# Optimization experiments

Measured on AMD Instinct MI355X. Metric: run time of the kernel, lower is better.

The kernel has to match this reference:

```python
import jax, jax.numpy as jnp
import numpy as np

CURV_BOUNDS = (-2.0, 2.0)
THRESH = 0.01   # |k| below this -> Euclidean branch
EPS = 1e-5

B, S, D = 4, 2048, 512


def setup_inputs() -> dict:
    key = jax.random.key(0)
    ks = jax.random.split(key, 8)
    x = jax.random.normal(ks[0], (B, S, D), jnp.float32)
    sc = 1.0 / np.sqrt(D)  # ~ nn.Linear default init scale
    Wq = jax.random.uniform(ks[1], (D, D), jnp.float32, -sc, sc)
    bq = jax.random.uniform(ks[2], (D,), jnp.float32, -sc, sc)
    Wk = jax.random.uniform(ks[3], (D, D), jnp.float32, -sc, sc)
    bk = jax.random.uniform(ks[4], (D,), jnp.float32, -sc, sc)
    Wv = jax.random.uniform(ks[5], (D, D), jnp.float32, -sc, sc)
    bv = jax.random.uniform(ks[6], (D,), jnp.float32, -sc, sc)
    curvature_raw = jnp.float32(0.5)   # init_curvature
    temperature = jnp.float32(1.0)
    mask = jnp.triu(jnp.ones((S, S), dtype=bool), 1)  # causal: True = masked out
    return {"x": x, "Wq": Wq, "bq": bq, "Wk": Wk, "bk": bk, "Wv": Wv,
            "bv": bv, "curvature_raw": curvature_raw,
            "temperature": temperature, "mask": mask}


def _curvature(raw):
    k_min, k_max = CURV_BOUNDS
    return k_min + (k_max - k_min) * (jnp.tanh(raw) + 1.0) / 2.0


def _project(u, k):
    # project_to_manifold: identity (euclid), Poincare-ball clip (k<0), sphere renorm (k>0)
    n = jnp.sqrt(jnp.sum(u * u, axis=-1, keepdims=True) + 1e-12)
    absk = jnp.abs(k)
    sk = jnp.sqrt(jnp.maximum(absk, EPS))
    max_norm = (1.0 - 1e-3) / sk                      # ball radius 1/sqrt(|k|)
    u_hyp = u * jnp.minimum(1.0, max_norm / n)
    u_sph = u / (n * sk)                              # sphere radius 1/sqrt(k)
    return jnp.where(absk < THRESH, u, jnp.where(k < 0, u_hyp, u_sph))


def reference(x, Wq, bq, Wk, bk, Wv, bv, curvature_raw, temperature, mask):
    k = _curvature(curvature_raw)
    q = x @ Wq.T + bq
    kk = x @ Wk.T + bk
    v = x @ Wv.T + bv
    qm = _project(q, k)
    km = _project(kk, k)

    # pairwise quantities without materializing [B,S,S,D]
    dots = jnp.einsum('bid,bjd->bij', qm, km)         # [B,S,S]
    qn2 = jnp.sum(qm * qm, axis=-1)                   # [B,S]
    kn2 = jnp.sum(km * km, axis=-1)                   # [B,S]
    diff2 = jnp.maximum(qn2[:, :, None] + kn2[:, None, :] - 2.0 * dots, 0.0)

    absk = jnp.abs(k)
    sk = jnp.sqrt(jnp.maximum(absk, EPS))

    d_euc = jnp.sqrt(diff2 + 1e-12)
    # hyperbolic (Poincare ball, c=|k|): acosh(1 + 2c|x-y|^2 / ((1-c|x|^2)(1-c|y|^2))) / sqrt(c)
    denom = jnp.maximum((1.0 - absk * qn2)[:, :, None] * (1.0 - absk * kn2)[:, None, :], EPS)
    arg = 1.0 + 2.0 * absk * diff2 / denom
    d_hyp = jnp.arccosh(jnp.maximum(arg, 1.0 + 1e-7)) / sk
    # spherical (radius 1/sqrt(k)): arccos(k * <x,y>) / sqrt(k)
    cosang = jnp.clip(absk * dots, -1.0 + 1e-7, 1.0 - 1e-7)
    d_sph = jnp.arccos(cosang) / sk

    dist = jnp.where(absk < THRESH, d_euc, jnp.where(k < 0, d_hyp, d_sph))

    scores = -dist / (temperature + 1e-8)
    scores = jnp.where(mask[None, :, :], -jnp.inf, scores)
    attention = jax.nn.softmax(scores, axis=-1)       # [B,S,S]
    output = jnp.einsum('bij,bjd->bid', attention, v) # [B,S,D]
    return output, attention
```

## Files before the change

### kernel.cpp

```cpp
#include <hip/hip_runtime.h>
#include <hip/hip_bf16.h>
#include <math.h>

typedef unsigned short u16;
typedef float float4e __attribute__((ext_vector_type(4)));
typedef short short8 __attribute__((ext_vector_type(8)));
typedef unsigned short ushort8 __attribute__((ext_vector_type(8)));
typedef unsigned short u16x4 __attribute__((ext_vector_type(4)));

#define SEQ 2048
#define DIM 512
#define NB  4

__device__ __forceinline__ float bf2f(u16 h) {
    return __uint_as_float(((unsigned)h) << 16);
}
__device__ __forceinline__ u16 f2bf(float f) {
    __hip_bfloat16 h = __float2bfloat16(f);
    return *reinterpret_cast<u16*>(&h);
}
__device__ __forceinline__ float curv_of(float raw) {
    return -2.0f + 2.0f * (tanhf(raw) + 1.0f);
}
__device__ __forceinline__ void gl_lds16(const u16* g, u16* lds) {
    __builtin_amdgcn_global_load_lds(
        (const __attribute__((address_space(1))) unsigned int*)g,
        (__attribute__((address_space(3))) unsigned int*)lds, 16, 0, 0);
}

__global__ __launch_bounds__(256) void cvt_all_kernel(
    const float* __restrict__ x, const float* __restrict__ Wq,
    const float* __restrict__ Wk, const float* __restrict__ Wv,
    u16* __restrict__ x_bf, u16* __restrict__ Wcat, float* __restrict__ lsum,
    float* __restrict__ outz)
{
    const int n_x = NB * SEQ * DIM, n_w = DIM * DIM;
    const int n_out = NB * SEQ * DIM;
    int gid = blockIdx.x * 256 + threadIdx.x;
    if (gid < NB * SEQ) lsum[gid] = 0.f;
    if (gid < n_out / 4) ((float4*)outz)[gid] = (float4){0.f, 0.f, 0.f, 0.f};
    int i4 = gid * 4;
    if (i4 < n_x) {
        float4 v = *(const float4*)&x[i4];
        u16x4 h = {f2bf(v.x), f2bf(v.y), f2bf(v.z), f2bf(v.w)};
        *(u16x4*)&x_bf[i4] = h;
    } else if (i4 < n_x + 3 * n_w) {
        int j = i4 - n_x;
        const float* W = (j < n_w) ? Wq : (j < 2 * n_w ? Wk : Wv);
        int off = j % n_w;
        float4 v = *(const float4*)&W[off];
        u16x4 h = {f2bf(v.x), f2bf(v.y), f2bf(v.z), f2bf(v.w)};
        *(u16x4*)&Wcat[j] = h;
    }
}

template<int MODE>
__global__ __launch_bounds__(256, 8) void gemm64_kernel(
    const u16* __restrict__ A, int lda, long long sA,
    const u16* __restrict__ Bt, int ldb, long long sB,
    void* __restrict__ Cv, int ldc, long long sC,
    u16* __restrict__ vT,
    float* __restrict__ lsum,
    const float* __restrict__ bq, const float* __restrict__ bk, const float* __restrict__ bv,
    const float* __restrict__ qn2v, const float* __restrict__ kn2v,
    const float* __restrict__ curvp, const float* __restrict__ tempp)
{
    int bx = blockIdx.x, bm = blockIdx.y, b = blockIdx.z;
    int bn = (MODE == 2) ? (bx & 7) : bx;
    int kp = (MODE == 2) ? (bx >> 3) : 0;
    if (MODE == 1 && bn > bm) return;

    __shared__ __align__(16) u16 As[64 * 64];
    __shared__ __align__(16) u16 Bs[64 * 64];

    int t = threadIdx.x, wave = t >> 6, lane = t & 63;
    int wr = wave >> 1, wc = wave & 1;
    int lrow = lane & 15, quad = lane >> 4;
    int srow = lane >> 3, sc = lane & 7;

    const u16* Ab = A + (size_t)b * sA + (size_t)(bm * 64) * lda;
    const u16* Bb = Bt + (size_t)b * sB + (size_t)(bn * 64) * ldb;

    float4e acc[2][2];
#pragma unroll
    for (int i = 0; i < 2; i++)
#pragma unroll
        for (int j = 0; j < 2; j++) acc[i][j] = (float4e){0.f, 0.f, 0.f, 0.f};

    int ktBeg = (MODE == 2) ? kp : 0;
    int ktEnd = (MODE == 2) ? (bm + 1) : 8;
    int ktStp = (MODE == 2) ? 2 : 1;

    for (int kt = ktBeg; kt < ktEnd; kt += ktStp) {
        int k0 = kt << 6;
        __syncthreads();
#pragma unroll
        for (int h = 0; h < 2; ++h) {
            int q = wave * 2 + h;
            int row = q * 8 + srow;
            int c = sc ^ (row & 7);
            gl_lds16(Ab + (size_t)row * lda + k0 + c * 8, &As[q * 512]);
            gl_lds16(Bb + (size_t)row * ldb + k0 + c * 8, &Bs[q * 512]);
        }
        __syncthreads();
#pragma unroll
        for (int s = 0; s < 2; ++s) {
            short8 af[2], bfr[2];
#pragma unroll
            for (int im = 0; im < 2; im++) {
                int R = wr * 32 + im * 16 + lrow;
                af[im] = *(const short8*)&As[R * 64 + (((s * 4 + quad) ^ (R & 7)) * 8)];
            }
#pragma unroll
            for (int in = 0; in < 2; in++) {
                int R = wc * 32 + in * 16 + lrow;
                bfr[in] = *(const short8*)&Bs[R * 64 + (((s * 4 + quad) ^ (R & 7)) * 8)];
            }
#pragma unroll
            for (int im = 0; im < 2; im++)
#pragma unroll
                for (int in = 0; in < 2; in++)
                    acc[im][in] = __builtin_amdgcn_mfma_f32_16x16x32_bf16(af[im], bfr[in], acc[im][in], 0, 0, 0);
        }
    }

    if (MODE == 0) {
        u16* Cb = (u16*)Cv;
#pragma unroll
        for (int im = 0; im < 2; im++)
#pragma unroll
            for (int in = 0; in < 2; in++) {
                int gi0 = bm * 64 + wr * 32 + im * 16 + quad * 4;
                int gj = bn * 64 + wc * 32 + in * 16 + lrow;
                float bias = (gj < 512) ? bq[gj] : (gj < 1024 ? bk[gj - 512] : bv[gj - 1024]);
                u16x4 pack;
#pragma unroll
                for (int r = 0; r < 4; r++) {
                    u16 hv = f2bf(acc[im][in][r] + bias);
                    Cb[(size_t)(gi0 + r) * ldc + gj] = hv;
                    pack[r] = hv;
                }
                if (gj >= 1024) {
                    int bb = gi0 >> 11, s = gi0 & 2047;
                    *(u16x4*)&vT[((size_t)bb * DIM + (gj - 1024)) * SEQ + s] = pack;
                }
            }
    } else if (MODE == 1) {
        float kv = curv_of(curvp[0]);
        float absk = fabsf(kv);
        float sk = sqrtf(fmaxf(absk, 1e-5f));
        float invT = 1.0f / (tempp[0] + 1e-8f);
        u16* Cb = (u16*)Cv + (size_t)b * sC;

        float psum[2][4];
#pragma unroll
        for (int im = 0; im < 2; im++)
#pragma unroll
            for (int r = 0; r < 4; r++) psum[im][r] = 0.f;

#pragma unroll
        for (int im = 0; im < 2; im++) {
#pragma unroll
            for (int r = 0; r < 4; r++) {
                int gi = bm * 64 + wr * 32 + im * 16 + quad * 4 + r;
                float qn = qn2v[b * SEQ + gi];
#pragma unroll
                for (int in = 0; in < 2; in++) {
                    int gj = bn * 64 + wc * 32 + in * 16 + lrow;
                    float kn = kn2v[b * SEQ + gj];
                    float dot = acc[im][in][r];
                    float diff2 = fmaxf(qn + kn - 2.f * dot, 0.f);
                    float dist;
                    if (absk < 0.01f) {
                        dist = sqrtf(diff2 + 1e-12f);
                    } else if (kv < 0.f) {
                        float denom = fmaxf((1.f - absk * qn) * (1.f - absk * kn), 1e-5f);
                        float arg = fmaxf(1.f + 2.f * absk * diff2 / denom, 1.f + 1e-7f);
                        dist = acoshf(arg) / sk;
                    } else {
                        float c = fminf(fmaxf(absk * dot, -1.f + 1e-7f), 1.f - 1e-7f);
                        dist = acosf(c) / sk;
                    }
                    float s = -dist * invT;
                    float e = (gj <= gi) ? __expf(s) : 0.f;
                    Cb[(size_t)gi * ldc + gj] = f2bf(e);
                    psum[im][r] += e;
                }
            }
        }
#pragma unroll
        for (int im = 0; im < 2; im++)
#pragma unroll
            for (int r = 0; r < 4; r++) {
                float v = psum[im][r];
                v += __shfl_xor(v, 1);
                v += __shfl_xor(v, 2);
                v += __shfl_xor(v, 4);
                v += __shfl_xor(v, 8);
                if (lrow == 0) {
                    int gi = bm * 64 + wr * 32 + im * 16 + quad * 4 + r;
                    atomicAdd(&lsum[b * SEQ + gi], v);
                }
            }
    } else {
        float* Cb = (float*)Cv + (size_t)b * sC;
#pragma unroll
        for (int im = 0; im < 2; im++)
#pragma unroll
            for (int r = 0; r < 4; r++) {
                int gi = bm * 64 + wr * 32 + im * 16 + quad * 4 + r;
                float invl = 1.0f / lsum[b * SEQ + gi];
#pragma unroll
                for (int in = 0; in < 2; in++) {
                    int gd = bn * 64 + wc * 32 + in * 16 + lrow;
                    atomicAdd(&Cb[(size_t)gi * ldc + gd], acc[im][in][r] * invl);
                }
            }
    }
}

__global__ __launch_bounds__(256) void project_kernel(
    const u16* __restrict__ qkvh,
    u16* __restrict__ qm, u16* __restrict__ km,
    float* __restrict__ qn2, float* __restrict__ kn2,
    const float* __restrict__ curvp)
{
    int wave = threadIdx.x >> 6, lane = threadIdx.x & 63;
    int r = blockIdx.x * 4 + wave;
    float kv = curv_of(curvp[0]);
    float absk = fabsf(kv);
    float sk = sqrtf(fmaxf(absk, 1e-5f));

    const u16* qrow = qkvh + (size_t)r * 1536;
    ushort8 qh = *(const ushort8*)&qrow[lane * 8];
    ushort8 kh = *(const ushort8*)&qrow[512 + lane * 8];

    float qv[8], kw[8];
    float sq = 0.f, s2 = 0.f;
#pragma unroll
    for (int e = 0; e < 8; e++) {
        qv[e] = bf2f(qh[e]); sq += qv[e] * qv[e];
        kw[e] = bf2f(kh[e]); s2 += kw[e] * kw[e];
    }
#pragma unroll
    for (int off = 1; off < 64; off <<= 1) {
        sq += __shfl_xor(sq, off);
        s2 += __shfl_xor(s2, off);
    }

    float sclq, sclk;
    {
        float nq = sqrtf(sq + 1e-12f);
        float nk = sqrtf(s2 + 1e-12f);
        if (absk < 0.01f) { sclq = 1.f; sclk = 1.f; }
        else if (kv < 0.f) {
            float mx = (1.0f - 1e-3f) / sk;
            sclq = fminf(1.f, mx / nq);
            sclk = fminf(1.f, mx / nk);
        } else {
            sclq = 1.f / (nq * sk);
            sclk = 1.f / (nk * sk);
        }
    }
    if (lane == 0) {
        qn2[r] = sq * sclq * sclq;
        kn2[r] = s2 * sclk * sclk;
    }
    ushort8 qo, ko;
#pragma unroll
    for (int e = 0; e < 8; e++) {
        qo[e] = f2bf(qv[e] * sclq);
        ko[e] = f2bf(kw[e] * sclk);
    }
    *(ushort8*)&qm[(size_t)r * 512 + lane * 8] = qo;
    *(ushort8*)&km[(size_t)r * 512 + lane * 8] = ko;
}

__global__ __launch_bounds__(256) void norm_attn_kernel(
    const u16* __restrict__ attnH, const float* __restrict__ lsum,
    float* __restrict__ attnF)
{
    int i = blockIdx.x, b = blockIdx.y, t = threadIdx.x;
    float inv = 1.0f / lsum[b * SEQ + i];
    const u16* rowh = attnH + ((size_t)b * SEQ + i) * SEQ;
    float* row = attnF + ((size_t)b * SEQ + i) * SEQ;
    int L = i + 1;
    int j0 = t * 8;
    float4 lo, hi;
    if (j0 + 8 <= L) {
        ushort8 h = *(const ushort8*)&rowh[j0];
        lo.x = bf2f(h[0]) * inv; lo.y = bf2f(h[1]) * inv;
        lo.z = bf2f(h[2]) * inv; lo.w = bf2f(h[3]) * inv;
        hi.x = bf2f(h[4]) * inv; hi.y = bf2f(h[5]) * inv;
        hi.z = bf2f(h[6]) * inv; hi.w = bf2f(h[7]) * inv;
    } else {
        float v[8];
#pragma unroll
        for (int e = 0; e < 8; e++)
            v[e] = (j0 + e < L) ? bf2f(rowh[j0 + e]) * inv : 0.f;
        lo = (float4){v[0], v[1], v[2], v[3]};
        hi = (float4){v[4], v[5], v[6], v[7]};
    }
    *(float4*)&row[j0] = lo;
    *(float4*)&row[j0 + 4] = hi;
}

extern "C" void kernel_launch(void* const* d_in, const int* in_sizes, int n_in,
                              void* d_out, int out_size, void* d_ws, size_t ws_size,
                              hipStream_t stream) {
    (void)in_sizes; (void)n_in; (void)out_size; (void)ws_size;

    const float* x    = (const float*)d_in[0];
    const float* Wq   = (const float*)d_in[1];
    const float* bq   = (const float*)d_in[2];
    const float* Wk   = (const float*)d_in[3];
    const float* bk   = (const float*)d_in[4];
    const float* Wv   = (const float*)d_in[5];
    const float* bv   = (const float*)d_in[6];
    const float* curv = (const float*)d_in[7];
    const float* temp = (const float*)d_in[8];

    float* out   = (float*)d_out;
    float* attnF = out + (size_t)NB * SEQ * DIM;

    char* ws = (char*)d_ws;
    u16*   x_bf  = (u16*)(ws + 0);
    u16*   Wcat  = (u16*)(ws + 8388608);
    u16*   qkvh  = (u16*)(ws + 9961472);
    u16*   qm    = (u16*)(ws + 35127296);
    u16*   km    = (u16*)(ws + 43515904);
    u16*   vT    = (u16*)(ws + 51904512);
    float* qn2   = (float*)(ws + 60293120);
    float* kn2   = (float*)(ws + 60325888);
    float* lsum  = (float*)(ws + 60358656);
    u16*   attnH = (u16*)(ws + 0);

    {
        int n_tot = (NB * SEQ * DIM + 3 * DIM * DIM) / 4;
        cvt_all_kernel<<<(n_tot + 255) / 256, 256, 0, stream>>>(x, Wq, Wk, Wv, x_bf, Wcat, lsum, out);
    }

    gemm64_kernel<0><<<dim3(1536 / 64, 8192 / 64, 1), 256, 0, stream>>>(
        x_bf, 512, 0, Wcat, 512, 0, (void*)qkvh, 1536, 0,
        vT, nullptr, bq, bk, bv, nullptr, nullptr, nullptr, nullptr);

    project_kernel<<<NB * SEQ / 4, 256, 0, stream>>>(qkvh, qm, km, qn2, kn2, curv);

    gemm64_kernel<1><<<dim3(SEQ / 64, SEQ / 64, NB), 256, 0, stream>>>(
        qm, 512, (long long)SEQ * DIM, km, 512, (long long)SEQ * DIM,
        (void*)attnH, SEQ, (long long)SEQ * SEQ,
        nullptr, lsum, nullptr, nullptr, nullptr, qn2, kn2, curv, temp);

    gemm64_kernel<2><<<dim3(2 * DIM / 64, SEQ / 64, NB), 256, 0, stream>>>(
        attnH, SEQ, (long long)SEQ * SEQ, vT, SEQ, (long long)DIM * SEQ,
        (void*)out, DIM, (long long)SEQ * DIM,
        nullptr, lsum, nullptr, nullptr, nullptr, nullptr, nullptr, nullptr, nullptr);

    norm_attn_kernel<<<dim3(SEQ, NB), 256, 0, stream>>>(attnH, lsum, attnF);
}
```

Before: 239.4 us.

## Switch GEMMs to 128x128 tiles with 32-wide K steps and add fast acos

```diff
diff --git a/kernel.cpp b/kernel.cpp
--- a/kernel.cpp
+++ b/kernel.cpp
@@ -21,6 +21,12 @@
 }
 __device__ __forceinline__ float curv_of(float raw) {
     return -2.0f + 2.0f * (tanhf(raw) + 1.0f);
+}
+__device__ __forceinline__ float fast_acos(float x) {
+    float ax = fabsf(x);
+    float r = sqrtf(fmaxf(1.f - ax, 0.f)) *
+              (1.5707288f + ax * (-0.2121144f + ax * (0.0742610f - 0.0187293f * ax)));
+    return (x < 0.f) ? (3.14159265f - r) : r;
 }
 __device__ __forceinline__ void gl_lds16(const u16* g, u16* lds) {
     __builtin_amdgcn_global_load_lds(
@@ -55,7 +61,7 @@
 }
 
 template<int MODE>
-__global__ __launch_bounds__(256, 8) void gemm64_kernel(
+__global__ __launch_bounds__(256) void gemm128_kernel(
     const u16* __restrict__ A, int lda, long long sA,
     const u16* __restrict__ Bt, int ldb, long long sB,
     void* __restrict__ Cv, int ldc, long long sC,
@@ -66,72 +72,69 @@
     const float* __restrict__ curvp, const float* __restrict__ tempp)
 {
     int bx = blockIdx.x, bm = blockIdx.y, b = blockIdx.z;
-    int bn = (MODE == 2) ? (bx & 7) : bx;
-    int kp = (MODE == 2) ? (bx >> 3) : 0;
+    int bn = (MODE == 2) ? (bx & 3) : bx;
+    int kp = (MODE == 2) ? (bx >> 2) : 0;
     if (MODE == 1 && bn > bm) return;
 
-    __shared__ __align__(16) u16 As[64 * 64];
-    __shared__ __align__(16) u16 Bs[64 * 64];
+    __shared__ __align__(16) u16 As[128 * 32];
+    __shared__ __align__(16) u16 Bs[128 * 32];
 
     int t = threadIdx.x, wave = t >> 6, lane = t & 63;
-    int wr = wave >> 1, wc = wave & 1;
+    int wm = wave >> 1, wn = wave & 1;
     int lrow = lane & 15, quad = lane >> 4;
-    int srow = lane >> 3, sc = lane & 7;
-
-    const u16* Ab = A + (size_t)b * sA + (size_t)(bm * 64) * lda;
-    const u16* Bb = Bt + (size_t)b * sB + (size_t)(bn * 64) * ldb;
-
-    float4e acc[2][2];
-#pragma unroll
-    for (int i = 0; i < 2; i++)
-#pragma unroll
-        for (int j = 0; j < 2; j++) acc[i][j] = (float4e){0.f, 0.f, 0.f, 0.f};
+    int srow = lane >> 2, sch = lane & 3;
+
+    const u16* Ab = A + (size_t)b * sA + (size_t)(bm * 128) * lda;
+    const u16* Bb = Bt + (size_t)b * sB + (size_t)(bn * 128) * ldb;
+
+    float4e acc[4][4];
+#pragma unroll
+    for (int i = 0; i < 4; i++)
+#pragma unroll
+        for (int j = 0; j < 4; j++) acc[i][j] = (float4e){0.f, 0.f, 0.f, 0.f};
 
     int ktBeg = (MODE == 2) ? kp : 0;
-    int ktEnd = (MODE == 2) ? (bm + 1) : 8;
+    int ktEnd = (MODE == 2) ? ((bm + 1) * 4) : 16;
     int ktStp = (MODE == 2) ? 2 : 1;
 
     for (int kt = ktBeg; kt < ktEnd; kt += ktStp) {
-        int k0 = kt << 6;
+        int k0 = kt << 5;
         __syncthreads();
 #pragma unroll
         for (int h = 0; h < 2; ++h) {
-            int q = wave * 2 + h;
-            int row = q * 8 + srow;
-            int c = sc ^ (row & 7);
-            gl_lds16(Ab + (size_t)row * lda + k0 + c * 8, &As[q * 512]);
-            gl_lds16(Bb + (size_t)row * ldb + k0 + c * 8, &Bs[q * 512]);
+            int row = wave * 16 + srow + h * 64;
+            int c = sch ^ (row & 3);
+            gl_lds16(Ab + (size_t)row * lda + k0 + c * 8, &As[(wave * 16 + h * 64) * 32]);
+            gl_lds16(Bb + (size_t)row * ldb + k0 + c * 8, &Bs[(wave * 16 + h * 64) * 32]);
         }
         __syncthreads();
-#pragma unroll
-        for (int s = 0; s < 2; ++s) {
-            short8 af[2], bfr[2];
-#pragma unroll
-            for (int im = 0; im < 2; im++) {
-                int R = wr * 32 + im * 16 + lrow;
-                af[im] = *(const short8*)&As[R * 64 + (((s * 4 + quad) ^ (R & 7)) * 8)];
-            }
-#pragma unroll
-            for (int in = 0; in < 2; in++) {
-                int R = wc * 32 + in * 16 + lrow;
-                bfr[in] = *(const short8*)&Bs[R * 64 + (((s * 4 + quad) ^ (R & 7)) * 8)];
-            }
-#pragma unroll
-            for (int im = 0; im < 2; im++)
-#pragma unroll
-                for (int in = 0; in < 2; in++)
-                    acc[im][in] = __builtin_amdgcn_mfma_f32_16x16x32_bf16(af[im], bfr[in], acc[im][in], 0, 0, 0);
-        }
+
+        short8 af[4], bfr[4];
+#pragma unroll
+        for (int im = 0; im < 4; im++) {
+            int R = wm * 64 + im * 16 + lrow;
+            af[im] = *(const short8*)&As[R * 32 + ((quad ^ (R & 3)) * 8)];
+        }
+#pragma unroll
+        for (int in = 0; in < 4; in++) {
+            int R = wn * 64 + in * 16 + lrow;
+            bfr[in] = *(const short8*)&Bs[R * 32 + ((quad ^ (R & 3)) * 8)];
+        }
+#pragma unroll
+        for (int im = 0; im < 4; im++)
+#pragma unroll
+            for (int in = 0; in < 4; in++)
+                acc[im][in] = __builtin_amdgcn_mfma_f32_16x16x32_bf16(af[im], bfr[in], acc[im][in], 0, 0, 0);
     }
 
     if (MODE == 0) {
         u16* Cb = (u16*)Cv;
 #pragma unroll
-        for (int im = 0; im < 2; im++)
-#pragma unroll
-            for (int in = 0; in < 2; in++) {
-                int gi0 = bm * 64 + wr * 32 + im * 16 + quad * 4;
-                int gj = bn * 64 + wc * 32 + in * 16 + lrow;
+        for (int im = 0; im < 4; im++)
+#pragma unroll
+            for (int in = 0; in < 4; in++) {
+                int gi0 = bm * 128 + wm * 64 + im * 16 + quad * 4;
+                int gj = bn * 128 + wn * 64 + in * 16 + lrow;
                 float bias = (gj < 512) ? bq[gj] : (gj < 1024 ? bk[gj - 512] : bv[gj - 1024]);
                 u16x4 pack;
 #pragma unroll
@@ -149,24 +152,25 @@
         float kv = curv_of(curvp[0]);
         float absk = fabsf(kv);
         float sk = sqrtf(fmaxf(absk, 1e-5f));
+        float invsk = 1.0f / sk;
         float invT = 1.0f / (tempp[0] + 1e-8f);
         u16* Cb = (u16*)Cv + (size_t)b * sC;
 
-        float psum[2][4];
-#pragma unroll
-        for (int im = 0; im < 2; im++)
+        float psum[4][4];
+#pragma unroll
+        for (int im = 0; im < 4; im++)
 #pragma unroll
             for (int r = 0; r < 4; r++) psum[im][r] = 0.f;
 
 #pragma unroll
-        for (int im = 0; im < 2; im++) {
+        for (int im = 0; im < 4; im++) {
 #pragma unroll
             for (int r = 0; r < 4; r++) {
-                int gi = bm * 64 + wr * 32 + im * 16 + quad * 4 + r;
+                int gi = bm * 128 + wm * 64 + im * 16 + quad * 4 + r;
                 float qn = qn2v[b * SEQ + gi];
 #pragma unroll
-                for (int in = 0; in < 2; in++) {
-                    int gj = bn * 64 + wc * 32 + in * 16 + lrow;
+                for (int in = 0; in < 4; in++) {
+                    int gj = bn * 128 + wn * 64 + in * 16 + lrow;
                     float kn = kn2v[b * SEQ + gj];
                     float dot = acc[im][in][r];
                     float diff2 = fmaxf(qn + kn - 2.f * dot, 0.f);
@@ -176,10 +180,10 @@
                     } else if (kv < 0.f) {
                         float denom = fmaxf((1.f - absk * qn) * (1.f - absk * kn), 1e-5f);
                         float arg = fmaxf(1.f + 2.f * absk * diff2 / denom, 1.f + 1e-7f);
-                        dist = acoshf(arg) / sk;
+                        dist = acoshf(arg) * invsk;
                     } else {
                         float c = fminf(fmaxf(absk * dot, -1.f + 1e-7f), 1.f - 1e-7f);
-                        dist = acosf(c) / sk;
+                        dist = fast_acos(c) * invsk;
                     }
                     float s = -dist * invT;
                     float e = (gj <= gi) ? __expf(s) : 0.f;
@@ -189,7 +193,7 @@
             }
         }
 #pragma unroll
-        for (int im = 0; im < 2; im++)
+        for (int im = 0; im < 4; im++)
 #pragma unroll
             for (int r = 0; r < 4; r++) {
                 float v = psum[im][r];
@@ -198,21 +202,21 @@
                 v += __shfl_xor(v, 4);
                 v += __shfl_xor(v, 8);
                 if (lrow == 0) {
-                    int gi = bm * 64 + wr * 32 + im * 16 + quad * 4 + r;
+                    int gi = bm * 128 + wm * 64 + im * 16 + quad * 4 + r;
                     atomicAdd(&lsum[b * SEQ + gi], v);
                 }
             }
     } else {
         float* Cb = (float*)Cv + (size_t)b * sC;
 #pragma unroll
-        for (int im = 0; im < 2; im++)
+        for (int im = 0; im < 4; im++)
 #pragma unroll
             for (int r = 0; r < 4; r++) {
-                int gi = bm * 64 + wr * 32 + im * 16 + quad * 4 + r;
+                int gi = bm * 128 + wm * 64 + im * 16 + quad * 4 + r;
                 float invl = 1.0f / lsum[b * SEQ + gi];
 #pragma unroll
-                for (int in = 0; in < 2; in++) {
-                    int gd = bn * 64 + wc * 32 + in * 16 + lrow;
+                for (int in = 0; in < 4; in++) {
+                    int gd = bn * 128 + wn * 64 + in * 16 + lrow;
                     atomicAdd(&Cb[(size_t)gi * ldc + gd], acc[im][in][r] * invl);
                 }
             }
@@ -340,18 +344,18 @@
         cvt_all_kernel<<<(n_tot + 255) / 256, 256, 0, stream>>>(x, Wq, Wk, Wv, x_bf, Wcat, lsum, out);
     }
 
-    gemm64_kernel<0><<<dim3(1536 / 64, 8192 / 64, 1), 256, 0, stream>>>(
+    gemm128_kernel<0><<<dim3(1536 / 128, 8192 / 128, 1), 256, 0, stream>>>(
         x_bf, 512, 0, Wcat, 512, 0, (void*)qkvh, 1536, 0,
         vT, nullptr, bq, bk, bv, nullptr, nullptr, nullptr, nullptr);
 
     project_kernel<<<NB * SEQ / 4, 256, 0, stream>>>(qkvh, qm, km, qn2, kn2, curv);
 
-    gemm64_kernel<1><<<dim3(SEQ / 64, SEQ / 64, NB), 256, 0, stream>>>(
+    gemm128_kernel<1><<<dim3(SEQ / 128, SEQ / 128, NB), 256, 0, stream>>>(
         qm, 512, (long long)SEQ * DIM, km, 512, (long long)SEQ * DIM,
         (void*)attnH, SEQ, (long long)SEQ * SEQ,
         nullptr, lsum, nullptr, nullptr, nullptr, qn2, kn2, curv, temp);
 
-    gemm64_kernel<2><<<dim3(2 * DIM / 64, SEQ / 64, NB), 256, 0, stream>>>(
+    gemm128_kernel<2><<<dim3(2 * DIM / 128, SEQ / 128, NB), 256, 0, stream>>>(
         attnH, SEQ, (long long)SEQ * SEQ, vT, SEQ, (long long)DIM * SEQ,
         (void*)out, DIM, (long long)SEQ * DIM,
         nullptr, lsum, nullptr, nullptr, nullptr, nullptr, nullptr, nullptr, nullptr);
```

Measured after the change: 279.9 us. 1.17x slower.

## Fuse fp32-to-bf16 conversion into QKV GEMM and drop split-K atomics in PV

Applied to the files above, without the earlier changes.

```diff
diff --git a/kernel.cpp b/kernel.cpp
--- a/kernel.cpp
+++ b/kernel.cpp
@@ -22,36 +22,105 @@
 __device__ __forceinline__ float curv_of(float raw) {
     return -2.0f + 2.0f * (tanhf(raw) + 1.0f);
 }
+__device__ __forceinline__ float fast_acos(float x) {
+    float ax = fabsf(x);
+    float r = sqrtf(fmaxf(1.f - ax, 0.f)) *
+              (1.5707288f + ax * (-0.2121144f + ax * (0.0742610f - 0.0187293f * ax)));
+    return (x < 0.f) ? (3.14159265f - r) : r;
+}
 __device__ __forceinline__ void gl_lds16(const u16* g, u16* lds) {
     __builtin_amdgcn_global_load_lds(
         (const __attribute__((address_space(1))) unsigned int*)g,
         (__attribute__((address_space(3))) unsigned int*)lds, 16, 0, 0);
 }
 
-__global__ __launch_bounds__(256) void cvt_all_kernel(
-    const float* __restrict__ x, const float* __restrict__ Wq,
-    const float* __restrict__ Wk, const float* __restrict__ Wv,
-    u16* __restrict__ x_bf, u16* __restrict__ Wcat, float* __restrict__ lsum,
-    float* __restrict__ outz)
+__global__ __launch_bounds__(256, 4) void qkv_kernel(
+    const float* __restrict__ xf,
+    const float* __restrict__ Wq, const float* __restrict__ Wk, const float* __restrict__ Wv,
+    const float* __restrict__ bq, const float* __restrict__ bk, const float* __restrict__ bv,
+    u16* __restrict__ C, u16* __restrict__ vT)
 {
-    const int n_x = NB * SEQ * DIM, n_w = DIM * DIM;
-    const int n_out = NB * SEQ * DIM;
-    int gid = blockIdx.x * 256 + threadIdx.x;
-    if (gid < NB * SEQ) lsum[gid] = 0.f;
-    if (gid < n_out / 4) ((float4*)outz)[gid] = (float4){0.f, 0.f, 0.f, 0.f};
-    int i4 = gid * 4;
-    if (i4 < n_x) {
-        float4 v = *(const float4*)&x[i4];
-        u16x4 h = {f2bf(v.x), f2bf(v.y), f2bf(v.z), f2bf(v.w)};
-        *(u16x4*)&x_bf[i4] = h;
-    } else if (i4 < n_x + 3 * n_w) {
-        int j = i4 - n_x;
-        const float* W = (j < n_w) ? Wq : (j < 2 * n_w ? Wk : Wv);
-        int off = j % n_w;
-        float4 v = *(const float4*)&W[off];
-        u16x4 h = {f2bf(v.x), f2bf(v.y), f2bf(v.z), f2bf(v.w)};
-        *(u16x4*)&Wcat[j] = h;
-    }
+    int bn = blockIdx.x, bm = blockIdx.y;
+
+    __shared__ __align__(16) u16 As[64 * 64];
+    __shared__ __align__(16) u16 Bs[64 * 64];
+
+    int t = threadIdx.x, wave = t >> 6, lane = t & 63;
+    int wr = wave >> 1, wc = wave & 1;
+    int lrow = lane & 15, quad = lane >> 4;
+    int srow = lane >> 3, sc = lane & 7;
+
+    const float* Af = xf + (size_t)(bm * 64) * 512;
+    const float* Wsel = (bn < 8) ? Wq : (bn < 16 ? Wk : Wv);
+    const float* Bf = Wsel + (size_t)((bn & 7) * 64) * 512;
+
+    float4e acc[2][2];
+#pragma unroll
+    for (int i = 0; i < 2; i++)
+#pragma unroll
+        for (int j = 0; j < 2; j++) acc[i][j] = (float4e){0.f, 0.f, 0.f, 0.f};
+
+    for (int kt = 0; kt < 8; ++kt) {
+        int k0 = kt << 6;
+        __syncthreads();
+#pragma unroll
+        for (int h = 0; h < 2; ++h) {
+            int q = wave * 2 + h;
+            int row = q * 8 + srow;
+            int c = sc ^ srow;
+            const float* ga = Af + (size_t)row * 512 + k0 + c * 8;
+            float4 a0 = *(const float4*)ga, a1 = *(const float4*)(ga + 4);
+            const float* gb = Bf + (size_t)row * 512 + k0 + c * 8;
+            float4 b0 = *(const float4*)gb, b1 = *(const float4*)(gb + 4);
+            ushort8 ha, hb;
+            ha[0] = f2bf(a0.x); ha[1] = f2bf(a0.y); ha[2] = f2bf(a0.z); ha[3] = f2bf(a0.w);
+            ha[4] = f2bf(a1.x); ha[5] = f2bf(a1.y); ha[6] = f2bf(a1.z); ha[7] = f2bf(a1.w);
+            hb[0] = f2bf(b0.x); hb[1] = f2bf(b0.y); hb[2] = f2bf(b0.z); hb[3] = f2bf(b0.w);
+            hb[4] = f2bf(b1.x); hb[5] = f2bf(b1.y); hb[6] = f2bf(b1.z); hb[7] = f2bf(b1.w);
+            *(ushort8*)&As[(size_t)row * 64 + sc * 8] = ha;
+            *(ushort8*)&Bs[(size_t)row * 64 + sc * 8] = hb;
+        }
+        __syncthreads();
+#pragma unroll
+        for (int s = 0; s < 2; ++s) {
+            short8 af[2], bfr[2];
+#pragma unroll
+            for (int im = 0; im < 2; im++) {
+                int R = wr * 32 + im * 16 + lrow;
+                af[im] = *(const short8*)&As[R * 64 + (((s * 4 + quad) ^ (R & 7)) * 8)];
+            }
+#pragma unroll
+            for (int in = 0; in < 2; in++) {
+                int R = wc * 32 + in * 16 + lrow;
+                bfr[in] = *(const short8*)&Bs[R * 64 + (((s * 4 + quad) ^ (R & 7)) * 8)];
+            }
+#pragma unroll
+            for (int im = 0; im < 2; im++)
+#pragma unroll
+                for (int in = 0; in < 2; in++)
+                    acc[im][in] = __builtin_amdgcn_mfma_f32_16x16x32_bf16(af[im], bfr[in], acc[im][in], 0, 0, 0);
+        }
+    }
+
+#pragma unroll
+    for (int im = 0; im < 2; im++)
+#pragma unroll
+        for (int in = 0; in < 2; in++) {
+            int gi0 = bm * 64 + wr * 32 + im * 16 + quad * 4;
+            int gj = bn * 64 + wc * 32 + in * 16 + lrow;
+            float bias = (gj < 512) ? bq[gj] : (gj < 1024 ? bk[gj - 512] : bv[gj - 1024]);
+            u16x4 pack;
+#pragma unroll
+            for (int r = 0; r < 4; r++) {
+                u16 hv = f2bf(acc[im][in][r] + bias);
+                C[(size_t)(gi0 + r) * 1536 + gj] = hv;
+                pack[r] = hv;
+            }
+            if (gj >= 1024) {
+                int bb = gi0 >> 11, s = gi0 & 2047;
+                *(u16x4*)&vT[((size_t)bb * DIM + (gj - 1024)) * SEQ + s] = pack;
+            }
+        }
 }
 
 template<int MODE>
@@ -59,15 +128,12 @@
     const u16* __restrict__ A, int lda, long long sA,
     const u16* __restrict__ Bt, int ldb, long long sB,
     void* __restrict__ Cv, int ldc, long long sC,
-    u16* __restrict__ vT,
     float* __restrict__ lsum,
-    const float* __restrict__ bq, const float* __restrict__ bk, const float* __restrict__ bv,
     const float* __restrict__ qn2v, const float* __restrict__ kn2v,
     const float* __restrict__ curvp, const float* __restrict__ tempp)
 {
-    int bx = blockIdx.x, bm = blockIdx.y, b = blockIdx.z;
-    int bn = (MODE == 2) ? (bx & 7) : bx;
-    int kp = (MODE == 2) ? (bx >> 3) : 0;
+    int bn = blockIdx.x, b = blockIdx.z;
+    int bm = (MODE == 2) ? (gridDim.y - 1 - blockIdx.y) : blockIdx.y;
     if (MODE == 1 && bn > bm) return;
 
     __shared__ __align__(16) u16 As[64 * 64];
@@ -87,18 +153,16 @@
 #pragma unroll
         for (int j = 0; j < 2; j++) acc[i][j] = (float4e){0.f, 0.f, 0.f, 0.f};
 
-    int ktBeg = (MODE == 2) ? kp : 0;
-    int ktEnd = (MODE == 2) ? (bm + 1) : 8;
-    int ktStp = (MODE == 2) ? 2 : 1;
-
-    for (int kt = ktBeg; kt < ktEnd; kt += ktStp) {
+    int kIters = (MODE == 2) ? (bm + 1) : 8;
+
+    for (int kt = 0; kt < kIters; ++kt) {
         int k0 = kt << 6;
         __syncthreads();
 #pragma unroll
         for (int h = 0; h < 2; ++h) {
             int q = wave * 2 + h;
             int row = q * 8 + srow;
-            int c = sc ^ (row & 7);
+            int c = sc ^ srow;
             gl_lds16(Ab + (size_t)row * lda + k0 + c * 8, &As[q * 512]);
             gl_lds16(Bb + (size_t)row * ldb + k0 + c * 8, &Bs[q * 512]);
         }
@@ -124,31 +188,11 @@
         }
     }
 
-    if (MODE == 0) {
-        u16* Cb = (u16*)Cv;
-#pragma unroll
-        for (int im = 0; im < 2; im++)
-#pragma unroll
-            for (int in = 0; in < 2; in++) {
-                int gi0 = bm * 64 + wr * 32 + im * 16 + quad * 4;
-                int gj = bn * 64 + wc * 32 + in * 16 + lrow;
-                float bias = (gj < 512) ? bq[gj] : (gj < 1024 ? bk[gj - 512] : bv[gj - 1024]);
-                u16x4 pack;
-#pragma unroll
-                for (int r = 0; r < 4; r++) {
-                    u16 hv = f2bf(acc[im][in][r] + bias);
-                    Cb[(size_t)(gi0 + r) * ldc + gj] = hv;
-                    pack[r] = hv;
-                }
-                if (gj >= 1024) {
-                    int bb = gi0 >> 11, s = gi0 & 2047;
-                    *(u16x4*)&vT[((size_t)bb * DIM + (gj - 1024)) * SEQ + s] = pack;
-                }
-            }
-    } else if (MODE == 1) {
+    if (MODE == 1) {
         float kv = curv_of(curvp[0]);
         float absk = fabsf(kv);
         float sk = sqrtf(fmaxf(absk, 1e-5f));
+        float invsk = 1.0f / sk;
         float invT = 1.0f / (tempp[0] + 1e-8f);
         u16* Cb = (u16*)Cv + (size_t)b * sC;
 
@@ -176,10 +220,10 @@
                     } else if (kv < 0.f) {
                         float denom = fmaxf((1.f - absk * qn) * (1.f - absk * kn), 1e-5f);
                         float arg = fmaxf(1.f + 2.f * absk * diff2 / denom, 1.f + 1e-7f);
-                        dist = acoshf(arg) / sk;
+                        dist = acoshf(arg) * invsk;
                     } else {
                         float c = fminf(fmaxf(absk * dot, -1.f + 1e-7f), 1.f - 1e-7f);
-                        dist = acosf(c) / sk;
+                        dist = fast_acos(c) * invsk;
                     }
                     float s = -dist * invT;
                     float e = (gj <= gi) ? __expf(s) : 0.f;
@@ -213,7 +257,7 @@
 #pragma unroll
                 for (int in = 0; in < 2; in++) {
                     int gd = bn * 64 + wc * 32 + in * 16 + lrow;
-                    atomicAdd(&Cb[(size_t)gi * ldc + gd], acc[im][in][r] * invl);
+                    Cb[(size_t)gi * ldc + gd] = acc[im][in][r] * invl;
                 }
             }
     }
@@ -223,8 +267,11 @@
     const u16* __restrict__ qkvh,
     u16* __restrict__ qm, u16* __restrict__ km,
     float* __restrict__ qn2, float* __restrict__ kn2,
+    float* __restrict__ lsum,
     const float* __restrict__ curvp)
 {
+    if (threadIdx.x < 4) lsum[blockIdx.x * 4 + threadIdx.x] = 0.f;
+
     int wave = threadIdx.x >> 6, lane = threadIdx.x & 63;
     int r = blockIdx.x * 4 + wave;
     float kv = curv_of(curvp[0]);
@@ -324,37 +371,29 @@
     float* attnF = out + (size_t)NB * SEQ * DIM;
 
     char* ws = (char*)d_ws;
-    u16*   x_bf  = (u16*)(ws + 0);
-    u16*   Wcat  = (u16*)(ws + 8388608);
-    u16*   qkvh  = (u16*)(ws + 9961472);
-    u16*   qm    = (u16*)(ws + 35127296);
-    u16*   km    = (u16*)(ws + 43515904);
-    u16*   vT    = (u16*)(ws + 51904512);
-    float* qn2   = (float*)(ws + 60293120);
-    float* kn2   = (float*)(ws + 60325888);
-    float* lsum  = (float*)(ws + 60358656);
+    u16*   qkvh  = (u16*)(ws + 0);
+    u16*   qm    = (u16*)(ws + 33554432);
+    u16*   km    = (u16*)(ws + 41943040);
+    u16*   vT    = (u16*)(ws + 50331648);
+    float* qn2   = (float*)(ws + 58720256);
+    float* kn2   = (float*)(ws + 58753024);
+    float* lsum  = (float*)(ws + 58785792);
     u16*   attnH = (u16*)(ws + 0);
 
-    {
-        int n_tot = (NB * SEQ * DIM + 3 * DIM * DIM) / 4;
-        cvt_all_kernel<<<(n_tot + 255) / 256, 256, 0, stream>>>(x, Wq, Wk, Wv, x_bf, Wcat, lsum, out);
-    }
-
-    gemm64_kernel<0><<<dim3(1536 / 64, 8192 / 64, 1), 256, 0, stream>>>(
-        x_bf, 512, 0, Wcat, 512, 0, (void*)qkvh, 1536, 0,
-        vT, nullptr, bq, bk, bv, nullptr, nullptr, nullptr, nullptr);
-
-    project_kernel<<<NB * SEQ / 4, 256, 0, stream>>>(qkvh, qm, km, qn2, kn2, curv);
+    qkv_kernel<<<dim3(1536 / 64, 8192 / 64, 1), 256, 0, stream>>>(
+        x, Wq, Wk, Wv, bq, bk, bv, qkvh, vT);
+
+    project_kernel<<<NB * SEQ / 4, 256, 0, stream>>>(qkvh, qm, km, qn2, kn2, lsum, curv);
 
     gemm64_kernel<1><<<dim3(SEQ / 64, SEQ / 64, NB), 256, 0, stream>>>(
         qm, 512, (long long)SEQ * DIM, km, 512, (long long)SEQ * DIM,
         (void*)attnH, SEQ, (long long)SEQ * SEQ,
-        nullptr, lsum, nullptr, nullptr, nullptr, qn2, kn2, curv, temp);
-
-    gemm64_kernel<2><<<dim3(2 * DIM / 64, SEQ / 64, NB), 256, 0, stream>>>(
+        lsum, qn2, kn2, curv, temp);
+
+    gemm64_kernel<2><<<dim3(DIM / 64, SEQ / 64, NB), 256, 0, stream>>>(
         attnH, SEQ, (long long)SEQ * SEQ, vT, SEQ, (long long)DIM * SEQ,
         (void*)out, DIM, (long long)SEQ * DIM,
-        nullptr, lsum, nullptr, nullptr, nullptr, nullptr, nullptr, nullptr, nullptr);
+        lsum, nullptr, nullptr, nullptr, nullptr);
 
     norm_attn_kernel<<<dim3(SEQ, NB), 256, 0, stream>>>(attnH, lsum, attnF);
 }
```

New measurement: 244.8 us. +2.3%, slower.
